# Kernel optimization log

Hardware: AMD Instinct MI355X
Metric: run time of the kernel (lower is better)

Reference implementation:

```python
import jax, jax.numpy as jnp
import numpy as np

N_NODES = 100000


def gcn_conv(x, edge_index, weight, num_nodes):
    """PyG GCNConv (bias=False): transform -> add self-loops -> sym-normalized scatter-add."""
    h = x @ weight  # [N, out]
    src, dst = edge_index[0], edge_index[1]
    loop = jnp.arange(num_nodes, dtype=src.dtype)
    src = jnp.concatenate([src, loop])
    dst = jnp.concatenate([dst, loop])
    ones = jnp.ones(src.shape[0], dtype=h.dtype)
    deg = jax.ops.segment_sum(ones, dst, num_segments=num_nodes)  # in-degree incl. self-loop
    dis = jnp.where(deg > 0, jax.lax.rsqrt(deg), 0.0)             # deg^-1/2, inf -> 0
    norm = dis[src] * dis[dst]                                    # [E+N]
    msg = norm[:, None] * h[src]                                  # gather + scale
    return jax.ops.segment_sum(msg, dst, num_segments=num_nodes)  # scatter-add


def setup_inputs() -> dict:
    key = jax.random.key(0)
    k1, k2, k3, k4 = jax.random.split(key, 4)
    x = jax.random.normal(k1, (N_NODES, 512), dtype=jnp.float32)
    edge_index = jax.random.randint(k2, (2, 3200000), 0, N_NODES, dtype=jnp.int64)
    weight1 = jax.random.normal(k3, (512, 16), dtype=jnp.float32) * 0.05
    weight2 = jax.random.normal(k4, (16, 16), dtype=jnp.float32) * 0.25
    return {"x": x, "edge_index": edge_index, "weight1": weight1, "weight2": weight2}


def reference(x, edge_index, weight1, weight2):
    n = x.shape[0]
    h = gcn_conv(x, edge_index, weight1, n)
    out = gcn_conv(h, edge_index, weight2, n)
    return out
```

## Files before the change

kernel.cpp:

```cpp
#include <hip/hip_runtime.h>
#include <hip/hip_bf16.h>


#define N_NODES 100000
#define F_IN 512
#define F_OUT 16
#define WS_PAD 516

__global__ void k_zero_i32(int* __restrict__ p, int n) {
    int i = blockIdx.x * blockDim.x + threadIdx.x;
    if (i < n) p[i] = 0;
}

__global__ void k_hist(const int* __restrict__ dst, int* __restrict__ deg, int E) {
    int e = blockIdx.x * blockDim.x + threadIdx.x;
    if (e < E) atomicAdd(&deg[dst[e]], 1);
}

__global__ void k_dis(const int* __restrict__ deg, float* __restrict__ dis, int n) {
    int i = blockIdx.x * blockDim.x + threadIdx.x;
    if (i < n) dis[i] = rsqrtf(1.0f + (float)deg[i]);
}

__global__ __launch_bounds__(512, 8) void k_gemm1(const float* __restrict__ x,
                                                  const float* __restrict__ W,
                                                  const float* __restrict__ dis,
                                                  float* __restrict__ hw,
                                                  float* __restrict__ accum,
                                                  int nrows) {
    __shared__ __align__(16) float Ws[F_OUT * WS_PAD];
    for (int i = threadIdx.x; i < F_IN * F_OUT; i += 512) {
        int k = i >> 4, o = i & 15;
        Ws[o * WS_PAD + k] = W[i];
    }
    __syncthreads();

    int l = threadIdx.x & 15;
    int r = blockIdx.x * 32 + (threadIdx.x >> 4);
    if (r >= nrows) return;

    const float4* xr = (const float4*)(x + (size_t)r * F_IN);
    const float* wrow = Ws + l * WS_PAD;
    float acc0 = 0.0f, acc1 = 0.0f;

#pragma unroll
    for (int half = 0; half < 2; ++half) {
        float4 v0 = xr[half * 64 + 0 * 16 + l];
        float4 v1 = xr[half * 64 + 1 * 16 + l];
        float4 v2 = xr[half * 64 + 2 * 16 + l];
        float4 v3 = xr[half * 64 + 3 * 16 + l];
        const float* wb = wrow + half * 256;
#pragma unroll
        for (int t = 0; t < 16; ++t) {
            float4 wa = *(const float4*)(wb + t * 4);
            float4 wc = *(const float4*)(wb + 64 + t * 4);
            acc0 = fmaf(__shfl(v0.x, t, 16), wa.x, acc0);
            acc0 = fmaf(__shfl(v0.y, t, 16), wa.y, acc0);
            acc0 = fmaf(__shfl(v0.z, t, 16), wa.z, acc0);
            acc0 = fmaf(__shfl(v0.w, t, 16), wa.w, acc0);
            acc1 = fmaf(__shfl(v1.x, t, 16), wc.x, acc1);
            acc1 = fmaf(__shfl(v1.y, t, 16), wc.y, acc1);
            acc1 = fmaf(__shfl(v1.z, t, 16), wc.z, acc1);
            acc1 = fmaf(__shfl(v1.w, t, 16), wc.w, acc1);
        }
#pragma unroll
        for (int t = 0; t < 16; ++t) {
            float4 wa = *(const float4*)(wb + 128 + t * 4);
            float4 wc = *(const float4*)(wb + 192 + t * 4);
            acc0 = fmaf(__shfl(v2.x, t, 16), wa.x, acc0);
            acc0 = fmaf(__shfl(v2.y, t, 16), wa.y, acc0);
            acc0 = fmaf(__shfl(v2.z, t, 16), wa.z, acc0);
            acc0 = fmaf(__shfl(v2.w, t, 16), wa.w, acc0);
            acc1 = fmaf(__shfl(v3.x, t, 16), wc.x, acc1);
            acc1 = fmaf(__shfl(v3.y, t, 16), wc.y, acc1);
            acc1 = fmaf(__shfl(v3.z, t, 16), wc.z, acc1);
            acc1 = fmaf(__shfl(v3.w, t, 16), wc.w, acc1);
        }
    }
    float hv = dis[r] * (acc0 + acc1);
    size_t o = (size_t)r * 16 + l;
    hw[o] = hv;
    accum[o] = hv;
}

__global__ __launch_bounds__(256) void k_gemm2(const float* __restrict__ S1,
                                               const float* __restrict__ W,
                                               const float* __restrict__ dis,
                                               float* __restrict__ hw2,
                                               float* __restrict__ accum,
                                               int nrows) {
    __shared__ float Ws[F_OUT * 17];
    if (threadIdx.x < 256) {
        int i = threadIdx.x;
        int k = i >> 4, o = i & 15;
        Ws[o * 17 + k] = W[i];
    }
    __syncthreads();
    int l = threadIdx.x & 15;
    int r = blockIdx.x * 16 + (threadIdx.x >> 4);
    if (r >= nrows) return;
    float dr = dis[r];
    float av = dr * S1[(size_t)r * 16 + l];
    const float* wrow = Ws + l * 17;
    float acc = 0.0f;
#pragma unroll
    for (int t = 0; t < 16; ++t) {
        float xv = __shfl(av, t, 16);
        acc = fmaf(xv, wrow[t], acc);
    }
    float hv = dr * acc;
    size_t o = (size_t)r * 16 + l;
    hw2[o] = hv;
    accum[o] = hv;
}

__global__ __launch_bounds__(256) void k_scatter(const int* __restrict__ src,
                                                 const int* __restrict__ dst,
                                                 const float* __restrict__ hw,
                                                 float* __restrict__ accum, int E) {
    int gid = blockIdx.x * 256 + threadIdx.x;
    int e = gid >> 4;
    if (e >= E) return;
    int c = gid & 15;
    int s = src[e];
    int d = dst[e];
    float v = hw[(size_t)s * 16 + c];
    unsafeAtomicAdd(&accum[(size_t)d * 16 + c], v);
}

__global__ void k_scale(float* __restrict__ out, const float* __restrict__ dis, int total) {
    int t = blockIdx.x * blockDim.x + threadIdx.x;
    if (t >= total) return;
    out[t] *= dis[t >> 4];
}

extern "C" void kernel_launch(void* const* d_in, const int* in_sizes, int n_in,
                              void* d_out, int out_size, void* d_ws, size_t ws_size,
                              hipStream_t stream) {
    const float* x  = (const float*)d_in[0];
    const int*   ei = (const int*)d_in[1];
    const float* W1 = (const float*)d_in[2];
    const float* W2 = (const float*)d_in[3];
    float* out = (float*)d_out;

    const int N = N_NODES;
    const int E = in_sizes[1] / 2;
    const int* src = ei;
    const int* dst = ei + E;
    const int B = 256;
    const int NC = N * F_OUT;

    float* dis  = (float*)d_ws;
    float* bufA = dis + N;
    float* bufB = bufA + (size_t)N * 16;
    int*   deg  = (int*)(bufB + (size_t)N * 16);

    k_zero_i32<<<(N + B - 1) / B, B, 0, stream>>>(deg, N);
    k_hist<<<(E + B - 1) / B, B, 0, stream>>>(dst, deg, E);
    k_dis<<<(N + B - 1) / B, B, 0, stream>>>(deg, dis, N);

    k_gemm1<<<(N + 31) / 32, 512, 0, stream>>>(x, W1, dis, bufA, bufB, N);
    {
        long long threads = (long long)E * 16;
        k_scatter<<<(unsigned)((threads + B - 1) / B), B, 0, stream>>>(src, dst, bufA, bufB, E);
    }

    k_gemm2<<<(N + 15) / 16, B, 0, stream>>>(bufB, W2, dis, bufA, out, N);
    {
        long long threads = (long long)E * 16;
        k_scatter<<<(unsigned)((threads + B - 1) / B), B, 0, stream>>>(src, dst, bufA, out, E);
    }
    k_scale<<<(NC + B - 1) / B, B, 0, stream>>>(out, dis, NC);
}
```

Before: 861.3 us.

## Restructure GEMM1 so each thread pair computes one row's full output

After: 801.4 us. 1.07x faster.

```diff
diff --git a/kernel.cpp b/kernel.cpp
--- a/kernel.cpp
+++ b/kernel.cpp
@@ -5,7 +5,6 @@
 #define N_NODES 100000
 #define F_IN 512
 #define F_OUT 16
-#define WS_PAD 516
 
 __global__ void k_zero_i32(int* __restrict__ p, int n) {
     int i = blockIdx.x * blockDim.x + threadIdx.x;
@@ -22,65 +21,87 @@
     if (i < n) dis[i] = rsqrtf(1.0f + (float)deg[i]);
 }
 
-__global__ __launch_bounds__(512, 8) void k_gemm1(const float* __restrict__ x,
-                                                  const float* __restrict__ W,
-                                                  const float* __restrict__ dis,
-                                                  float* __restrict__ hw,
-                                                  float* __restrict__ accum,
-                                                  int nrows) {
-    __shared__ __align__(16) float Ws[F_OUT * WS_PAD];
-    for (int i = threadIdx.x; i < F_IN * F_OUT; i += 512) {
-        int k = i >> 4, o = i & 15;
-        Ws[o * WS_PAD + k] = W[i];
+__global__ __launch_bounds__(256) void k_gemm1(const float* __restrict__ x,
+                                               const float* __restrict__ W,
+                                               const float* __restrict__ dis,
+                                               float* __restrict__ hw,
+                                               float* __restrict__ accum,
+                                               int nrows) {
+    __shared__ __align__(16) float Ws[F_IN * F_OUT];
+    {
+        const float4* Wg = (const float4*)W;
+        float4* Ws4 = (float4*)Ws;
+        for (int i = threadIdx.x; i < (F_IN * F_OUT) / 4; i += 256) Ws4[i] = Wg[i];
     }
     __syncthreads();
 
-    int l = threadIdx.x & 15;
-    int r = blockIdx.x * 32 + (threadIdx.x >> 4);
+    int t = blockIdx.x * 256 + threadIdx.x;
+    int r = t >> 1;
+    int h = t & 1;
     if (r >= nrows) return;
 
-    const float4* xr = (const float4*)(x + (size_t)r * F_IN);
-    const float* wrow = Ws + l * WS_PAD;
-    float acc0 = 0.0f, acc1 = 0.0f;
+    const float4* xr = (const float4*)(x + (size_t)r * F_IN) + h * 64;
+    const float4* Wb = (const float4*)Ws + h * 1024;
+
+    float acc[16];
+#pragma unroll
+    for (int o = 0; o < 16; ++o) acc[o] = 0.0f;
+
+    for (int c = 0; c < 16; ++c) {
+        float4 xv0 = xr[c * 4 + 0];
+        float4 xv1 = xr[c * 4 + 1];
+        float4 xv2 = xr[c * 4 + 2];
+        float4 xv3 = xr[c * 4 + 3];
+        float xa[16] = {xv0.x, xv0.y, xv0.z, xv0.w,
+                        xv1.x, xv1.y, xv1.z, xv1.w,
+                        xv2.x, xv2.y, xv2.z, xv2.w,
+                        xv3.x, xv3.y, xv3.z, xv3.w};
+        const float4* wk = Wb + c * 64;
+#pragma unroll
+        for (int kk = 0; kk < 16; ++kk) {
+            float4 w0 = wk[kk * 4 + 0];
+            float4 w1 = wk[kk * 4 + 1];
+            float4 w2 = wk[kk * 4 + 2];
+            float4 w3 = wk[kk * 4 + 3];
+            float xk = xa[kk];
+            acc[0]  = fmaf(xk, w0.x, acc[0]);
+            acc[1]  = fmaf(xk, w0.y, acc[1]);
+            acc[2]  = fmaf(xk, w0.z, acc[2]);
+            acc[3]  = fmaf(xk, w0.w, acc[3]);
+            acc[4]  = fmaf(xk, w1.x, acc[4]);
+            acc[5]  = fmaf(xk, w1.y, acc[5]);
+            acc[6]  = fmaf(xk, w1.z, acc[6]);
+            acc[7]  = fmaf(xk, w1.w, acc[7]);
+            acc[8]  = fmaf(xk, w2.x, acc[8]);
+            acc[9]  = fmaf(xk, w2.y, acc[9]);
+            acc[10] = fmaf(xk, w2.z, acc[10]);
+            acc[11] = fmaf(xk, w2.w, acc[11]);
+            acc[12] = fmaf(xk, w3.x, acc[12]);
+            acc[13] = fmaf(xk, w3.y, acc[13]);
+            acc[14] = fmaf(xk, w3.z, acc[14]);
+            acc[15] = fmaf(xk, w3.w, acc[15]);
+        }
+    }
 
 #pragma unroll
-    for (int half = 0; half < 2; ++half) {
-        float4 v0 = xr[half * 64 + 0 * 16 + l];
-        float4 v1 = xr[half * 64 + 1 * 16 + l];
-        float4 v2 = xr[half * 64 + 2 * 16 + l];
-        float4 v3 = xr[half * 64 + 3 * 16 + l];
-        const float* wb = wrow + half * 256;
-#pragma unroll
-        for (int t = 0; t < 16; ++t) {
-            float4 wa = *(const float4*)(wb + t * 4);
-            float4 wc = *(const float4*)(wb + 64 + t * 4);
-            acc0 = fmaf(__shfl(v0.x, t, 16), wa.x, acc0);
-            acc0 = fmaf(__shfl(v0.y, t, 16), wa.y, acc0);
-            acc0 = fmaf(__shfl(v0.z, t, 16), wa.z, acc0);
-            acc0 = fmaf(__shfl(v0.w, t, 16), wa.w, acc0);
-            acc1 = fmaf(__shfl(v1.x, t, 16), wc.x, acc1);
-            acc1 = fmaf(__shfl(v1.y, t, 16), wc.y, acc1);
-            acc1 = fmaf(__shfl(v1.z, t, 16), wc.z, acc1);
-            acc1 = fmaf(__shfl(v1.w, t, 16), wc.w, acc1);
-        }
-#pragma unroll
-        for (int t = 0; t < 16; ++t) {
-            float4 wa = *(const float4*)(wb + 128 + t * 4);
-            float4 wc = *(const float4*)(wb + 192 + t * 4);
-            acc0 = fmaf(__shfl(v2.x, t, 16), wa.x, acc0);
-            acc0 = fmaf(__shfl(v2.y, t, 16), wa.y, acc0);
-            acc0 = fmaf(__shfl(v2.z, t, 16), wa.z, acc0);
-            acc0 = fmaf(__shfl(v2.w, t, 16), wa.w, acc0);
-            acc1 = fmaf(__shfl(v3.x, t, 16), wc.x, acc1);
-            acc1 = fmaf(__shfl(v3.y, t, 16), wc.y, acc1);
-            acc1 = fmaf(__shfl(v3.z, t, 16), wc.z, acc1);
-            acc1 = fmaf(__shfl(v3.w, t, 16), wc.w, acc1);
-        }
-    }
-    float hv = dis[r] * (acc0 + acc1);
-    size_t o = (size_t)r * 16 + l;
-    hw[o] = hv;
-    accum[o] = hv;
+    for (int o = 0; o < 16; ++o) acc[o] += __shfl_xor(acc[o], 1);
+
+    float dr = dis[r];
+    float s0 = h ? acc[8]  : acc[0];
+    float s1 = h ? acc[9]  : acc[1];
+    float s2 = h ? acc[10] : acc[2];
+    float s3 = h ? acc[11] : acc[3];
+    float s4 = h ? acc[12] : acc[4];
+    float s5 = h ? acc[13] : acc[5];
+    float s6 = h ? acc[14] : acc[6];
+    float s7 = h ? acc[15] : acc[7];
+    float4 p0 = make_float4(dr * s0, dr * s1, dr * s2, dr * s3);
+    float4 p1 = make_float4(dr * s4, dr * s5, dr * s6, dr * s7);
+    size_t base = (size_t)r * 16 + h * 8;
+    *(float4*)(hw + base)        = p0;
+    *(float4*)(hw + base + 4)    = p1;
+    *(float4*)(accum + base)     = p0;
+    *(float4*)(accum + base + 4) = p1;
 }
 
 __global__ __launch_bounds__(256) void k_gemm2(const float* __restrict__ S1,
@@ -159,7 +180,7 @@
     k_hist<<<(E + B - 1) / B, B, 0, stream>>>(dst, deg, E);
     k_dis<<<(N + B - 1) / B, B, 0, stream>>>(deg, dis, N);
 
-    k_gemm1<<<(N + 31) / 32, 512, 0, stream>>>(x, W1, dis, bufA, bufB, N);
+    k_gemm1<<<(2 * N + 255) / 256, 256, 0, stream>>>(x, W1, dis, bufA, bufB, N);
     {
         long long threads = (long long)E * 16;
         k_scatter<<<(unsigned)((threads + B - 1) / B), B, 0, stream>>>(src, dst, bufA, bufB, E);
```
